# Optimization experiments

Hardware: AMD Instinct MI355X
Metric: run time of the kernel (lower is better)

## Reference

```python
import jax, jax.numpy as jnp
import numpy as np

B, S, I, H, O = 128, 512, 1024, 1024, 1024


def setup_inputs() -> dict:
    key = jax.random.key(0)
    ks = jax.random.split(key, 11)
    s = 0.02  # small init scale to keep exp/log-gate math stable
    return {
        "x": jax.random.normal(ks[0], (B, S, I), dtype=jnp.float32),
        "Wf": jax.random.normal(ks[1], (I + H, H), dtype=jnp.float32) * s,
        "bf": jax.random.normal(ks[2], (H,), dtype=jnp.float32) * s,
        "Wi": jax.random.normal(ks[3], (I + H, H), dtype=jnp.float32) * s,
        "bi": jax.random.normal(ks[4], (H,), dtype=jnp.float32) * s,
        "Wc": jax.random.normal(ks[5], (I + H, H), dtype=jnp.float32) * s,
        "bc": jax.random.normal(ks[6], (H,), dtype=jnp.float32) * s,
        "Wo": jax.random.normal(ks[7], (I + H, H), dtype=jnp.float32) * s,
        "bo": jax.random.normal(ks[8], (H,), dtype=jnp.float32) * s,
        "Wout": jax.random.normal(ks[9], (H, O), dtype=jnp.float32) * s,
        "bout": jax.random.normal(ks[10], (O,), dtype=jnp.float32) * s,
    }


def reference(x, Wf, bf, Wi, bi, Wc, bc, Wo, bo, Wout, bout):
    batch, seq_len, _ = x.shape
    hid = Wf.shape[1]

    def step(carry, x_t):
        h, c, n, m = carry  # each [B, H]
        comb = jnp.concatenate([x_t, h], axis=1)  # [B, I+H]
        f_log = comb @ Wf + bf
        i_log = comb @ Wi + bi
        m_new = jnp.maximum(f_log + m, i_log)  # stabilizer
        i_t = jnp.exp(i_log - m_new)
        f_t = jnp.exp(f_log + m - m_new)
        c_hat = jnp.tanh(comb @ Wc + bc)
        o_t = jax.nn.sigmoid(comb @ Wo + bo)
        c_new = f_t * c + i_t * c_hat
        n_new = f_t * n + i_t
        h_new = o_t * (c_new / (n_new + 1e-8))
        out = h_new @ Wout + bout  # [B, O]
        return (h_new, c_new, n_new, m_new), out

    init = tuple(jnp.zeros((batch, hid), x.dtype) for _ in range(4))
    (h, c, n, m), outs = jax.lax.scan(step, init, jnp.swapaxes(x, 0, 1))
    outputs = jnp.swapaxes(outs, 0, 1)  # [B, S, O]
    return outputs, h, c, n, m
```

## Files before the change

### kernel.cpp

```cpp
#include <hip/hip_runtime.h>
#include <cstddef>

#define B_ 128
#define S_ 512
#define I_ 1024
#define H_ 1024
#define G4_ 4096

typedef __attribute__((ext_vector_type(8))) short bf16x8;
typedef __attribute__((ext_vector_type(4))) float f32x4;
typedef unsigned short u16;
typedef unsigned int   u32;

__device__ inline u16 bf16_rn(float x) {
  return (u16)((__float_as_uint(x) + 0x8000u) >> 16);
}
__device__ inline u16 bf16_hi_rem(float x, float& rem) {
  const u32 hb = (__float_as_uint(x) + 0x8000u) & 0xFFFF0000u;
  rem = x - __uint_as_float(hb);
  return (u16)(hb >> 16);
}

__global__ __launch_bounds__(256) void k_zero(float* __restrict__ p, int n) {
  int i = blockIdx.x * 256 + threadIdx.x;
  if (i < n) p[i] = 0.0f;
}

__global__ __launch_bounds__(256) void k_wt(
    const float* __restrict__ Wf, const float* __restrict__ Wi,
    const float* __restrict__ Wc, const float* __restrict__ Wo,
    float* __restrict__ WT)
{
  const int gid = blockIdx.x * 256 + threadIdx.x;
  const int j4 = gid >> 12;
  const int s  = gid & 4095;
  const int ki = s >> 6, g = (s >> 4) & 3, kq = s & 15;
  const int k  = kq * 64 + ki;
  const float* Wg = (g == 0) ? Wf : (g == 1) ? Wi : (g == 2) ? Wc : Wo;
  const float4 v = *(const float4*)(Wg + (size_t)(I_ + k) * H_ + j4 * 4);
  *(float4*)(WT + (size_t)gid * 4) = v;
}

__global__ __launch_bounds__(256) void k_tr(
    const float* __restrict__ Wf, const float* __restrict__ Wi,
    const float* __restrict__ Wc, const float* __restrict__ Wo,
    const float* __restrict__ Wout,
    u16* __restrict__ Wxt_hi, u16* __restrict__ Wxt_lo,
    u16* __restrict__ Wot_hi, u16* __restrict__ Wot_lo)
{
  __shared__ float T_[64][65];
  const int kt = blockIdx.x, jt = blockIdx.y, z = blockIdx.z;
  const float* src = (z == 0) ? Wf : (z == 1) ? Wi : (z == 2) ? Wc
                     : (z == 3) ? Wo : Wout;
  u16* dh = (z < 4) ? Wxt_hi : Wot_hi;
  u16* dl = (z < 4) ? Wxt_lo : Wot_lo;
  const int nbase = (z < 4) ? (z * 1024 + jt * 64) : (jt * 64);
  const int tid = threadIdx.x;

#pragma unroll
  for (int it = 0; it < 4; ++it) {
    const int idx = it * 1024 + tid * 4;
    const int a = idx >> 6, c = idx & 63;
    const float4 v = *(const float4*)(src + (size_t)(kt * 64 + a) * 1024 + jt * 64 + c);
    T_[a][c] = v.x; T_[a][c + 1] = v.y; T_[a][c + 2] = v.z; T_[a][c + 3] = v.w;
  }
  __syncthreads();
#pragma unroll
  for (int it = 0; it < 16; ++it) {
    const int idx = it * 256 + tid;
    const int j = idx >> 6, k = idx & 63;
    const float xv = T_[k][j];
    float rem;
    const u16 hi = bf16_hi_rem(xv, rem);
    const u16 lo = bf16_rn(rem);
    const size_t o = (size_t)(nbase + j) * 1024 + kt * 64 + k;
    dh[o] = hi; dl[o] = lo;
  }
}

__global__ __launch_bounds__(256) void k_bias(
    const float* __restrict__ b0, const float* __restrict__ b1,
    const float* __restrict__ b2, const float* __restrict__ b3,
    float* __restrict__ b4)
{
  const int i = blockIdx.x * 256 + threadIdx.x;
  const int g = i >> 10;
  const float* s = (g == 0) ? b0 : (g == 1) ? b1 : (g == 2) ? b2 : b3;
  b4[i] = s[i & 1023];
}

__global__ __launch_bounds__(256) void k_xsplit(
    const float* __restrict__ x, u16* __restrict__ xh, u16* __restrict__ xl, int t0)
{
  const int id = blockIdx.x * 256 + threadIdx.x;
  const int tl = blockIdx.y;
  const int b  = id >> 7;
  const int k8 = (id & 127) << 3;
  const float* s = x + ((size_t)b * 512 + (size_t)(t0 + tl)) * 1024 + k8;
  const float4 v0 = *(const float4*)(s);
  const float4 v1 = *(const float4*)(s + 4);
  const float vs[8] = {v0.x, v0.y, v0.z, v0.w, v1.x, v1.y, v1.z, v1.w};
  u32 hw[4], lw[4];
#pragma unroll
  for (int p = 0; p < 4; ++p) {
    float r0, r1;
    const u16 h0 = bf16_hi_rem(vs[2 * p], r0);
    const u16 h1 = bf16_hi_rem(vs[2 * p + 1], r1);
    hw[p] = (u32)h0 | ((u32)h1 << 16);
    lw[p] = (u32)bf16_rn(r0) | ((u32)bf16_rn(r1) << 16);
  }
  const size_t o = ((size_t)tl * 128 + b) * 1024 + k8;
  *(uint4*)(xh + o) = make_uint4(hw[0], hw[1], hw[2], hw[3]);
  *(uint4*)(xl + o) = make_uint4(lw[0], lw[1], lw[2], lw[3]);
}

template<int MODE>
__global__ __launch_bounds__(256) void k_gemm_mfma(
    const u16* __restrict__ Ahg, const u16* __restrict__ Alg,
    const u16* __restrict__ Bhg, const u16* __restrict__ Blg,
    const float* __restrict__ bias,
    float* __restrict__ C, int t0)
{
  __shared__ u16 Ah[4096], Al[4096], Bh[4096], Bl[4096];
  const int tid = threadIdx.x;
  const int n0  = blockIdx.x * 128;
  const int by  = blockIdx.y;

  const int w = tid >> 6, lane = tid & 63;
  const int wm = w >> 1, wn = w & 1;
  const int lr = lane & 15, lh = lane >> 4;

  f32x4 acc[4][4];
#pragma unroll
  for (int mi = 0; mi < 4; ++mi)
#pragma unroll
    for (int ni = 0; ni < 4; ++ni) acc[mi][ni] = (f32x4){0.f, 0.f, 0.f, 0.f};

  const int srow  = tid >> 1;
  const int sb    = (tid & 1) * 2;
  const int swz   = (srow >> 1) & 3;
  const int l0 = srow * 32 + ((sb ^ swz) << 3);
  const int l1 = srow * 32 + (((sb + 1) ^ swz) << 3);
  const size_t ga = (size_t)(by * 128 + srow) * 1024 + (sb << 3);
  const size_t gb = (size_t)(n0 + srow) * 1024 + (sb << 3);

  int aoff[4], boff[4];
#pragma unroll
  for (int mi = 0; mi < 4; ++mi) {
    const int R = wm * 64 + mi * 16 + lr;
    aoff[mi] = R * 32 + ((lh ^ ((R >> 1) & 3)) << 3);
  }
#pragma unroll
  for (int ni = 0; ni < 4; ++ni) {
    const int Rn = wn * 64 + ni * 16 + lr;
    boff[ni] = Rn * 32 + ((lh ^ ((Rn >> 1) & 3)) << 3);
  }

  for (int k0 = 0; k0 < 1024; k0 += 32) {
    const uint4 vah0 = *(const uint4*)(Ahg + ga + k0);
    const uint4 vah1 = *(const uint4*)(Ahg + ga + k0 + 8);
    const uint4 vbh0 = *(const uint4*)(Bhg + gb + k0);
    const uint4 vbh1 = *(const uint4*)(Bhg + gb + k0 + 8);
    uint4 val0, val1, vbl0, vbl1;
    if (MODE == 0) {
      val0 = *(const uint4*)(Alg + ga + k0);
      val1 = *(const uint4*)(Alg + ga + k0 + 8);
      vbl0 = *(const uint4*)(Blg + gb + k0);
      vbl1 = *(const uint4*)(Blg + gb + k0 + 8);
    }
    __syncthreads();
    *(uint4*)(Ah + l0) = vah0; *(uint4*)(Ah + l1) = vah1;
    *(uint4*)(Bh + l0) = vbh0; *(uint4*)(Bh + l1) = vbh1;
    if (MODE == 0) {
      *(uint4*)(Al + l0) = val0; *(uint4*)(Al + l1) = val1;
      *(uint4*)(Bl + l0) = vbl0; *(uint4*)(Bl + l1) = vbl1;
    }
    __syncthreads();

    bf16x8 ahf[4], alf[4];
#pragma unroll
    for (int mi = 0; mi < 4; ++mi) {
      ahf[mi] = *(const bf16x8*)(&Ah[aoff[mi]]);
      if (MODE == 0) alf[mi] = *(const bf16x8*)(&Al[aoff[mi]]);
    }
#pragma unroll
    for (int ni = 0; ni < 4; ++ni) {
      const bf16x8 bhf = *(const bf16x8*)(&Bh[boff[ni]]);
      bf16x8 blf;
      if (MODE == 0) blf = *(const bf16x8*)(&Bl[boff[ni]]);
#pragma unroll
      for (int mi = 0; mi < 4; ++mi) {
        acc[mi][ni] = __builtin_amdgcn_mfma_f32_16x16x32_bf16(ahf[mi], bhf, acc[mi][ni], 0, 0, 0);
        if (MODE == 0) {
          acc[mi][ni] = __builtin_amdgcn_mfma_f32_16x16x32_bf16(ahf[mi], blf, acc[mi][ni], 0, 0, 0);
          acc[mi][ni] = __builtin_amdgcn_mfma_f32_16x16x32_bf16(alf[mi], bhf, acc[mi][ni], 0, 0, 0);
        }
      }
    }
  }

#pragma unroll
  for (int ni = 0; ni < 4; ++ni) {
    const int n = n0 + wn * 64 + ni * 16 + lr;
    const float bv = bias[n];
#pragma unroll
    for (int mi = 0; mi < 4; ++mi) {
      const int rb = wm * 64 + mi * 16 + lh * 4;
#pragma unroll
      for (int q = 0; q < 4; ++q) {
        const int r = rb + q;
        const float v = acc[mi][ni][q] + bv;
        if (MODE == 0) C[((size_t)by * 128 + r) * 4096 + n] = v;
        else           C[((size_t)r * 512 + (size_t)(t0 + by)) * 1024 + n] = v;
      }
    }
  }
}

__global__ __launch_bounds__(512) void k_step2(
    const float* __restrict__ WT,
    const float* __restrict__ preC,
    const float* __restrict__ hT_in,
    float* __restrict__ hT_out,
    float* __restrict__ cb, float* __restrict__ nb, float* __restrict__ mb,
    u16* __restrict__ hAllH,
    int t_local)
{
  __shared__ float Wl[16384];
  const int tid = threadIdx.x;
  const int bid = blockIdx.x;
  const int j0  = bid * 4;

  const int w    = tid >> 6;
  const int lane = tid & 63;
  const int kq   = lane & 15;
  const int bq   = lane >> 4;
  const int b0   = w * 16 + bq * 4;

  const int jj = kq & 3, ib = kq >> 2;
  const int bc = b0 + ib;
  const int jc = j0 + jj;
  const int sIdx = jc * 128 + bc;

  const float* pre_t = preC + (size_t)t_local * (128 * 4096) + (size_t)bc * 4096 + jc;
  const float pf = pre_t[0];
  const float pi = pre_t[1024];
  const float pc = pre_t[2048];
  const float po = pre_t[3072];
  const float m_old = mb[sIdx];
  const float c_old = cb[sIdx];
  const float n_old = nb[sIdx];

  const float* wt = WT + (size_t)bid * 16384;
#pragma unroll
  for (int r = 0; r < 8; ++r) {
    const int idx = r * 512 + tid;
    *(float4*)(&Wl[idx * 4]) = *(const float4*)(wt + (size_t)idx * 4);
  }
  __syncthreads();

  float acc[4][16];
#pragma unroll
  for (int i = 0; i < 4; ++i)
#pragma unroll
    for (int c = 0; c < 16; ++c) acc[i][c] = 0.0f;

  const float* hbase = hT_in + (size_t)kq * (64 * 128) + b0;
  const float* wb0   = &Wl[kq * 4];

  float4 h_c = *(const float4*)(hbase);
  float4 h_n = *(const float4*)(hbase + 128);
  float4 wA = *(const float4*)(wb0 + 0);
  float4 wB = *(const float4*)(wb0 + 64);
  float4 wC = *(const float4*)(wb0 + 128);
  float4 wD = *(const float4*)(wb0 + 192);

#pragma unroll 2
  for (int ki = 0; ki < 64; ++ki) {
    const int kin = (ki + 1) & 63;
    const int ki2 = (ki + 2) & 63;
    const float4 h_p = *(const float4*)(hbase + ki2 * 128);
    const float4 nA = *(const float4*)(wb0 + kin * 256 + 0);
    const float4 nB = *(const float4*)(wb0 + kin * 256 + 64);
    const float4 nC = *(const float4*)(wb0 + kin * 256 + 128);
    const float4 nD = *(const float4*)(wb0 + kin * 256 + 192);
    const float av[4] = {h_c.x, h_c.y, h_c.z, h_c.w};
    const float wv[16] = {wA.x, wA.y, wA.z, wA.w, wB.x, wB.y, wB.z, wB.w,
                          wC.x, wC.y, wC.z, wC.w, wD.x, wD.y, wD.z, wD.w};
#pragma unroll
    for (int i = 0; i < 4; ++i)
#pragma unroll
      for (int c = 0; c < 16; ++c)
        acc[i][c] = fmaf(av[i], wv[c], acc[i][c]);
    h_c = h_n; h_n = h_p;
    wA = nA; wB = nB; wC = nC; wD = nD;
  }

#pragma unroll
  for (int i = 0; i < 4; ++i)
#pragma unroll
    for (int c = 0; c < 16; ++c) {
      float v = acc[i][c];
      v += __shfl_xor(v, 1);
      v += __shfl_xor(v, 2);
      v += __shfl_xor(v, 4);
      v += __shfl_xor(v, 8);
      acc[i][c] = v;
    }

  float f_in, i_in, cc_in, o_in;
#define PICK_CASE(KQ) \
  case KQ: f_in = acc[(KQ) >> 2][(KQ) & 3];        \
           i_in = acc[(KQ) >> 2][4 + ((KQ) & 3)];  \
           cc_in = acc[(KQ) >> 2][8 + ((KQ) & 3)]; \
           o_in = acc[(KQ) >> 2][12 + ((KQ) & 3)]; break;
  switch (kq) {
    PICK_CASE(0)  PICK_CASE(1)  PICK_CASE(2)  PICK_CASE(3)
    PICK_CASE(4)  PICK_CASE(5)  PICK_CASE(6)  PICK_CASE(7)
    PICK_CASE(8)  PICK_CASE(9)  PICK_CASE(10) PICK_CASE(11)
    PICK_CASE(12) PICK_CASE(13) PICK_CASE(14) PICK_CASE(15)
    default: f_in = i_in = cc_in = o_in = 0.0f; break;
  }
#undef PICK_CASE

  const float f_log = f_in + pf;
  const float i_log = i_in + pi;
  const float c_log = cc_in + pc;
  const float o_log = o_in + po;

  const float m_new = fmaxf(f_log + m_old, i_log);
  const float i_t   = expf(i_log - m_new);
  const float f_t   = expf(f_log + m_old - m_new);
  const float c_hat = tanhf(c_log);
  const float o_t   = 1.0f / (1.0f + expf(-o_log));
  const float c_new = f_t * c_old + i_t * c_hat;
  const float n_new = f_t * n_old + i_t;
  const float h_new = o_t * (c_new / (n_new + 1e-8f));

  cb[sIdx] = c_new;
  nb[sIdx] = n_new;
  mb[sIdx] = m_new;
  hT_out[sIdx] = h_new;
  hAllH[((size_t)t_local * 128 + bc) * 1024 + jc] = bf16_rn(h_new);
}

__global__ __launch_bounds__(256) void k_tail(
    const float* __restrict__ hT, const float* __restrict__ cbp,
    const float* __restrict__ nbp, const float* __restrict__ mbp,
    float* __restrict__ dst)
{
  const int gid = blockIdx.x * 256 + threadIdx.x;
  const int q = gid >> 17, rem = gid & 131071;
  const int b = rem >> 10, j = rem & 1023;
  const float* src = (q == 0) ? hT : (q == 1) ? cbp : (q == 2) ? nbp : mbp;
  dst[gid] = src[j * B_ + b];
}

extern "C" void kernel_launch(void* const* d_in, const int* in_sizes, int n_in,
                              void* d_out, int out_size, void* d_ws, size_t ws_size,
                              hipStream_t stream) {
  const float* x    = (const float*)d_in[0];
  const float* Wf   = (const float*)d_in[1];
  const float* bfv  = (const float*)d_in[2];
  const float* Wi   = (const float*)d_in[3];
  const float* biv  = (const float*)d_in[4];
  const float* Wc   = (const float*)d_in[5];
  const float* bcv  = (const float*)d_in[6];
  const float* Wo   = (const float*)d_in[7];
  const float* bov  = (const float*)d_in[8];
  const float* Wout = (const float*)d_in[9];
  const float* bout = (const float*)d_in[10];
  float* out = (float*)d_out;

  float* hT0 = (float*)d_ws;
  float* hT1 = hT0 + 131072;
  float* cb  = hT0 + 2 * 131072;
  float* nb  = hT0 + 3 * 131072;
  float* mb  = hT0 + 4 * 131072;
  float* WT  = hT0 + 5 * 131072;
  u16* Wxt_hi = (u16*)(WT + 4194304);
  u16* Wxt_lo = Wxt_hi + 4194304;
  u16* Wot_hi = Wxt_lo + 4194304;
  u16* Wot_lo = Wot_hi + 1048576;
  float* bias4  = (float*)(Wot_lo + 1048576);
  float* chunk0 = bias4 + 4096;

  const size_t fixedF = (size_t)5 * 131072 + 4194304
                      + 4194304
                      + 1048576
                      + 4096;
  const size_t perTF = (size_t)128 * 4096 + 3 * 65536;
  const size_t availF = (ws_size / 4 > fixedF) ? (ws_size / 4 - fixedF) : 0;
  int Tc = (int)(availF / perTF);
  if (Tc > S_) Tc = S_;
  if (Tc < 1)  Tc = 1;

  float* preC   = chunk0;
  u16*   xs_hi  = (u16*)(preC + (size_t)Tc * 524288);
  u16*   xs_lo  = xs_hi + (size_t)Tc * 131072;
  u16*   hAll_h = xs_lo + (size_t)Tc * 131072;

  k_zero<<<2560, 256, 0, stream>>>(hT0, 5 * 131072);
  k_wt<<<4096, 256, 0, stream>>>(Wf, Wi, Wc, Wo, WT);
  k_tr<<<dim3(16, 16, 5), 256, 0, stream>>>(Wf, Wi, Wc, Wo, Wout,
                                            Wxt_hi, Wxt_lo, Wot_hi, Wot_lo);
  k_bias<<<16, 256, 0, stream>>>(bfv, biv, bcv, bov, bias4);

  for (int t0 = 0; t0 < S_; t0 += Tc) {
    const int T = (S_ - t0 < Tc) ? (S_ - t0) : Tc;

    k_xsplit<<<dim3(64, T), 256, 0, stream>>>(x, xs_hi, xs_lo, t0);
    k_gemm_mfma<0><<<dim3(32, T), 256, 0, stream>>>(xs_hi, xs_lo, Wxt_hi, Wxt_lo,
                                                    bias4, preC, t0);
    for (int tl = 0; tl < T; ++tl) {
      const int tg = t0 + tl;
      const float* hin = (tg & 1) ? hT1 : hT0;
      float* hout      = (tg & 1) ? hT0 : hT1;
      k_step2<<<256, 512, 0, stream>>>(WT, preC, hin, hout,
                                       cb, nb, mb, hAll_h, tl);
    }
    k_gemm_mfma<1><<<dim3(8, T), 256, 0, stream>>>(hAll_h, hAll_h, Wot_hi, Wot_hi,
                                                   bout, out, t0);
  }

  k_tail<<<2048, 256, 0, stream>>>(hT0, cb, nb, mb, out + (size_t)B_ * S_ * H_);
}
```

Measured before the change: 16.59 ms.

## Replace FP32 recurrent step with split-bf16 MFMA and gate-interleaved weights

The per-timestep recurrent matmul (h @ W_h) moves from scalar FP32 FMA over weights staged in LDS to bf16 MFMA instructions. Three products (hi*hi, hi*lo, lo*hi) approximate FP32 accuracy. Weights are pre-split into hi/lo bf16 and interleaved by gate so each output column group holds f,i,c,o together, and the bias layout is changed to match. The hidden state is double-buffered as hi/lo bf16, and gates are gathered with lane shuffles. Precision drops slightly because the lo*lo term is omitted, and each block now reads its weights straight from global/L2 every step instead of staging them in LDS.

```diff
diff --git a/kernel.cpp b/kernel.cpp
--- a/kernel.cpp
+++ b/kernel.cpp
@@ -26,42 +26,29 @@
   if (i < n) p[i] = 0.0f;
 }
 
-__global__ __launch_bounds__(256) void k_wt(
-    const float* __restrict__ Wf, const float* __restrict__ Wi,
-    const float* __restrict__ Wc, const float* __restrict__ Wo,
-    float* __restrict__ WT)
-{
-  const int gid = blockIdx.x * 256 + threadIdx.x;
-  const int j4 = gid >> 12;
-  const int s  = gid & 4095;
-  const int ki = s >> 6, g = (s >> 4) & 3, kq = s & 15;
-  const int k  = kq * 64 + ki;
-  const float* Wg = (g == 0) ? Wf : (g == 1) ? Wi : (g == 2) ? Wc : Wo;
-  const float4 v = *(const float4*)(Wg + (size_t)(I_ + k) * H_ + j4 * 4);
-  *(float4*)(WT + (size_t)gid * 4) = v;
-}
-
 __global__ __launch_bounds__(256) void k_tr(
     const float* __restrict__ Wf, const float* __restrict__ Wi,
     const float* __restrict__ Wc, const float* __restrict__ Wo,
     const float* __restrict__ Wout,
     u16* __restrict__ Wxt_hi, u16* __restrict__ Wxt_lo,
-    u16* __restrict__ Wot_hi, u16* __restrict__ Wot_lo)
+    u16* __restrict__ Wot_hi, u16* __restrict__ Wot_lo,
+    u16* __restrict__ Wht_hi, u16* __restrict__ Wht_lo)
 {
   __shared__ float T_[64][65];
   const int kt = blockIdx.x, jt = blockIdx.y, z = blockIdx.z;
-  const float* src = (z == 0) ? Wf : (z == 1) ? Wi : (z == 2) ? Wc
-                     : (z == 3) ? Wo : Wout;
-  u16* dh = (z < 4) ? Wxt_hi : Wot_hi;
-  u16* dl = (z < 4) ? Wxt_lo : Wot_lo;
-  const int nbase = (z < 4) ? (z * 1024 + jt * 64) : (jt * 64);
+  const int g = (z < 4) ? z : (z - 5);
+  const float* src = (z == 4) ? Wout
+                   : (g == 0) ? Wf : (g == 1) ? Wi : (g == 2) ? Wc : Wo;
+  u16* dh = (z < 4) ? Wxt_hi : (z == 4) ? Wot_hi : Wht_hi;
+  u16* dl = (z < 4) ? Wxt_lo : (z == 4) ? Wot_lo : Wht_lo;
+  const int rowbase = ((z >= 5) ? I_ : 0) + kt * 64;
   const int tid = threadIdx.x;
 
 #pragma unroll
   for (int it = 0; it < 4; ++it) {
     const int idx = it * 1024 + tid * 4;
     const int a = idx >> 6, c = idx & 63;
-    const float4 v = *(const float4*)(src + (size_t)(kt * 64 + a) * 1024 + jt * 64 + c);
+    const float4 v = *(const float4*)(src + (size_t)(rowbase + a) * 1024 + jt * 64 + c);
     T_[a][c] = v.x; T_[a][c + 1] = v.y; T_[a][c + 2] = v.z; T_[a][c + 3] = v.w;
   }
   __syncthreads();
@@ -73,7 +60,9 @@
     float rem;
     const u16 hi = bf16_hi_rem(xv, rem);
     const u16 lo = bf16_rn(rem);
-    const size_t o = (size_t)(nbase + j) * 1024 + kt * 64 + k;
+    size_t o;
+    if (z == 4) o = (size_t)(jt * 64 + j) * 1024 + kt * 64 + k;
+    else        o = ((size_t)(jt * 64 + j) * 4 + g) * 1024 + kt * 64 + k;
     dh[o] = hi; dl[o] = lo;
   }
 }
@@ -84,9 +73,9 @@
     float* __restrict__ b4)
 {
   const int i = blockIdx.x * 256 + threadIdx.x;
-  const int g = i >> 10;
+  const int g = i & 3, j = i >> 2;
   const float* s = (g == 0) ? b0 : (g == 1) ? b1 : (g == 2) ? b2 : b3;
-  b4[i] = s[i & 1023];
+  b4[i] = s[j];
 }
 
 __global__ __launch_bounds__(256) void k_xsplit(
@@ -217,116 +206,69 @@
   }
 }
 
-__global__ __launch_bounds__(512) void k_step2(
-    const float* __restrict__ WT,
+__global__ __launch_bounds__(512) void k_step3(
+    const u16* __restrict__ Whh, const u16* __restrict__ Whl,
     const float* __restrict__ preC,
-    const float* __restrict__ hT_in,
-    float* __restrict__ hT_out,
+    const u16* __restrict__ hIh, const u16* __restrict__ hIl,
+    u16* __restrict__ hOh, u16* __restrict__ hOl,
+    float* __restrict__ hT,
     float* __restrict__ cb, float* __restrict__ nb, float* __restrict__ mb,
     u16* __restrict__ hAllH,
     int t_local)
 {
-  __shared__ float Wl[16384];
   const int tid = threadIdx.x;
   const int bid = blockIdx.x;
-  const int j0  = bid * 4;
-
-  const int w    = tid >> 6;
-  const int lane = tid & 63;
-  const int kq   = lane & 15;
-  const int bq   = lane >> 4;
-  const int b0   = w * 16 + bq * 4;
-
-  const int jj = kq & 3, ib = kq >> 2;
-  const int bc = b0 + ib;
-  const int jc = j0 + jj;
-  const int sIdx = jc * 128 + bc;
-
-  const float* pre_t = preC + (size_t)t_local * (128 * 4096) + (size_t)bc * 4096 + jc;
-  const float pf = pre_t[0];
-  const float pi = pre_t[1024];
-  const float pc = pre_t[2048];
-  const float po = pre_t[3072];
+  const int jt = bid >> 2, mq = bid & 3;
+  const int w = tid >> 6, lane = tid & 63;
+  const int mi = w & 1, nf = w >> 1;
+  const int lr = lane & 15, lh = lane >> 4;
+  const int rowb = mq * 32 + mi * 16;
+
+  const int G = lr & 3;
+  const int j = jt * 16 + nf * 4 + (lr >> 2);
+  const int b = rowb + lh * 4 + G;
+  const int sIdx = j * 128 + b;
+
+  const float4 pre4 = *(const float4*)(preC + (size_t)t_local * (128 * 4096)
+                                       + (size_t)b * 4096 + j * 4);
   const float m_old = mb[sIdx];
   const float c_old = cb[sIdx];
   const float n_old = nb[sIdx];
 
-  const float* wt = WT + (size_t)bid * 16384;
-#pragma unroll
-  for (int r = 0; r < 8; ++r) {
-    const int idx = r * 512 + tid;
-    *(float4*)(&Wl[idx * 4]) = *(const float4*)(wt + (size_t)idx * 4);
-  }
-  __syncthreads();
-
-  float acc[4][16];
-#pragma unroll
-  for (int i = 0; i < 4; ++i)
-#pragma unroll
-    for (int c = 0; c < 16; ++c) acc[i][c] = 0.0f;
-
-  const float* hbase = hT_in + (size_t)kq * (64 * 128) + b0;
-  const float* wb0   = &Wl[kq * 4];
-
-  float4 h_c = *(const float4*)(hbase);
-  float4 h_n = *(const float4*)(hbase + 128);
-  float4 wA = *(const float4*)(wb0 + 0);
-  float4 wB = *(const float4*)(wb0 + 64);
-  float4 wC = *(const float4*)(wb0 + 128);
-  float4 wD = *(const float4*)(wb0 + 192);
-
-#pragma unroll 2
-  for (int ki = 0; ki < 64; ++ki) {
-    const int kin = (ki + 1) & 63;
-    const int ki2 = (ki + 2) & 63;
-    const float4 h_p = *(const float4*)(hbase + ki2 * 128);
-    const float4 nA = *(const float4*)(wb0 + kin * 256 + 0);
-    const float4 nB = *(const float4*)(wb0 + kin * 256 + 64);
-    const float4 nC = *(const float4*)(wb0 + kin * 256 + 128);
-    const float4 nD = *(const float4*)(wb0 + kin * 256 + 192);
-    const float av[4] = {h_c.x, h_c.y, h_c.z, h_c.w};
-    const float wv[16] = {wA.x, wA.y, wA.z, wA.w, wB.x, wB.y, wB.z, wB.w,
-                          wC.x, wC.y, wC.z, wC.w, wD.x, wD.y, wD.z, wD.w};
-#pragma unroll
-    for (int i = 0; i < 4; ++i)
-#pragma unroll
-      for (int c = 0; c < 16; ++c)
-        acc[i][c] = fmaf(av[i], wv[c], acc[i][c]);
-    h_c = h_n; h_n = h_p;
-    wA = nA; wB = nB; wC = nC; wD = nD;
-  }
-
-#pragma unroll
-  for (int i = 0; i < 4; ++i)
-#pragma unroll
-    for (int c = 0; c < 16; ++c) {
-      float v = acc[i][c];
-      v += __shfl_xor(v, 1);
-      v += __shfl_xor(v, 2);
-      v += __shfl_xor(v, 4);
-      v += __shfl_xor(v, 8);
-      acc[i][c] = v;
-    }
-
-  float f_in, i_in, cc_in, o_in;
-#define PICK_CASE(KQ) \
-  case KQ: f_in = acc[(KQ) >> 2][(KQ) & 3];        \
-           i_in = acc[(KQ) >> 2][4 + ((KQ) & 3)];  \
-           cc_in = acc[(KQ) >> 2][8 + ((KQ) & 3)]; \
-           o_in = acc[(KQ) >> 2][12 + ((KQ) & 3)]; break;
-  switch (kq) {
-    PICK_CASE(0)  PICK_CASE(1)  PICK_CASE(2)  PICK_CASE(3)
-    PICK_CASE(4)  PICK_CASE(5)  PICK_CASE(6)  PICK_CASE(7)
-    PICK_CASE(8)  PICK_CASE(9)  PICK_CASE(10) PICK_CASE(11)
-    PICK_CASE(12) PICK_CASE(13) PICK_CASE(14) PICK_CASE(15)
-    default: f_in = i_in = cc_in = o_in = 0.0f; break;
-  }
-#undef PICK_CASE
-
-  const float f_log = f_in + pf;
-  const float i_log = i_in + pi;
-  const float c_log = cc_in + pc;
-  const float o_log = o_in + po;
+  const u16* aH = hIh + (size_t)(rowb + lr) * 1024 + lh * 8;
+  const u16* aL = hIl + (size_t)(rowb + lr) * 1024 + lh * 8;
+  const u16* bH = Whh + (size_t)(jt * 64 + nf * 16 + lr) * 1024 + lh * 8;
+  const u16* bL = Whl + (size_t)(jt * 64 + nf * 16 + lr) * 1024 + lh * 8;
+
+  f32x4 acc = {0.f, 0.f, 0.f, 0.f};
+#pragma unroll 4
+  for (int k0 = 0; k0 < 1024; k0 += 32) {
+    const bf16x8 ah = *(const bf16x8*)(aH + k0);
+    const bf16x8 al = *(const bf16x8*)(aL + k0);
+    const bf16x8 bh = *(const bf16x8*)(bH + k0);
+    const bf16x8 bl = *(const bf16x8*)(bL + k0);
+    acc = __builtin_amdgcn_mfma_f32_16x16x32_bf16(ah, bh, acc, 0, 0, 0);
+    acc = __builtin_amdgcn_mfma_f32_16x16x32_bf16(ah, bl, acc, 0, 0, 0);
+    acc = __builtin_amdgcn_mfma_f32_16x16x32_bf16(al, bh, acc, 0, 0, 0);
+  }
+
+  const float a0 = acc[0], a1 = acc[1], a2 = acc[2], a3 = acc[3];
+  const float s10 = __shfl_xor(a0, 1), s11 = __shfl_xor(a1, 1),
+              s12 = __shfl_xor(a2, 1), s13 = __shfl_xor(a3, 1);
+  const float s20 = __shfl_xor(a0, 2), s21 = __shfl_xor(a1, 2),
+              s22 = __shfl_xor(a2, 2), s23 = __shfl_xor(a3, 2);
+  const float s30 = __shfl_xor(a0, 3), s31 = __shfl_xor(a1, 3),
+              s32 = __shfl_xor(a2, 3), s33 = __shfl_xor(a3, 3);
+  float fv, iv, cv, ov;
+  if      (G == 0) { fv = a0;  iv = s10; cv = s20; ov = s30; }
+  else if (G == 1) { fv = s11; iv = a1;  cv = s31; ov = s21; }
+  else if (G == 2) { fv = s22; iv = s32; cv = a2;  ov = s12; }
+  else             { fv = s33; iv = s23; cv = s13; ov = a3;  }
+
+  const float f_log = fv + pre4.x;
+  const float i_log = iv + pre4.y;
+  const float c_log = cv + pre4.z;
+  const float o_log = ov + pre4.w;
 
   const float m_new = fmaxf(f_log + m_old, i_log);
   const float i_t   = expf(i_log - m_new);
@@ -340,8 +282,14 @@
   cb[sIdx] = c_new;
   nb[sIdx] = n_new;
   mb[sIdx] = m_new;
-  hT_out[sIdx] = h_new;
-  hAllH[((size_t)t_local * 128 + bc) * 1024 + jc] = bf16_rn(h_new);
+  hT[sIdx] = h_new;
+
+  float rem;
+  const u16 hh = bf16_hi_rem(h_new, rem);
+  const u16 hl = bf16_rn(rem);
+  hOh[(size_t)b * 1024 + j] = hh;
+  hOl[(size_t)b * 1024 + j] = hl;
+  hAllH[((size_t)t_local * 128 + b) * 1024 + j] = hh;
 }
 
 __global__ __launch_bounds__(256) void k_tail(
@@ -372,38 +320,50 @@
   const float* bout = (const float*)d_in[10];
   float* out = (float*)d_out;
 
-  float* hT0 = (float*)d_ws;
-  float* hT1 = hT0 + 131072;
-  float* cb  = hT0 + 2 * 131072;
-  float* nb  = hT0 + 3 * 131072;
-  float* mb  = hT0 + 4 * 131072;
-  float* WT  = hT0 + 5 * 131072;
-  u16* Wxt_hi = (u16*)(WT + 4194304);
+  float* base = (float*)d_ws;
+  float* hT = base;
+  float* cb = base + 131072;
+  float* nb = base + 2 * 131072;
+  float* mb = base + 3 * 131072;
+  u16* hH0h = (u16*)(base + 4 * 131072);
+  u16* hH0l = hH0h + 131072;
+  u16* hH1h = hH0l + 131072;
+  u16* hH1l = hH1h + 131072;
+  u16* Wxt_hi = (u16*)(base + 6 * 131072);
   u16* Wxt_lo = Wxt_hi + 4194304;
-  u16* Wot_hi = Wxt_lo + 4194304;
+  u16* Wht_hi = Wxt_lo + 4194304;
+  u16* Wht_lo = Wht_hi + 4194304;
+  u16* Wot_hi = Wht_lo + 4194304;
   u16* Wot_lo = Wot_hi + 1048576;
   float* bias4  = (float*)(Wot_lo + 1048576);
   float* chunk0 = bias4 + 4096;
 
-  const size_t fixedF = (size_t)5 * 131072 + 4194304
-                      + 4194304
-                      + 1048576
-                      + 4096;
+  const size_t fixedF = (size_t)6 * 131072
+                      + 4 * 2097152
+                      + 2 * 524288 / 2 * 2
+                      ;
+  const size_t fixedF2 = (size_t)6 * 131072
+                       + ((size_t)4 * 4194304 + 2 * 1048576) / 2
+                       + 4096;
   const size_t perTF = (size_t)128 * 4096 + 3 * 65536;
-  const size_t availF = (ws_size / 4 > fixedF) ? (ws_size / 4 - fixedF) : 0;
+  const size_t availF = (ws_size / 4 > fixedF2) ? (ws_size / 4 - fixedF2) : 0;
   int Tc = (int)(availF / perTF);
   if (Tc > S_) Tc = S_;
   if (Tc < 1)  Tc = 1;
+  (void)fixedF;
 
   float* preC   = chunk0;
   u16*   xs_hi  = (u16*)(preC + (size_t)Tc * 524288);
   u16*   xs_lo  = xs_hi + (size_t)Tc * 131072;
   u16*   hAll_h = xs_lo + (size_t)Tc * 131072;
 
-  k_zero<<<2560, 256, 0, stream>>>(hT0, 5 * 131072);
-  k_wt<<<4096, 256, 0, stream>>>(Wf, Wi, Wc, Wo, WT);
-  k_tr<<<dim3(16, 16, 5), 256, 0, stream>>>(Wf, Wi, Wc, Wo, Wout,
-                                            Wxt_hi, Wxt_lo, Wot_hi, Wot_lo);
+  u16* hHi[2] = {hH0h, hH1h};
+  u16* hLo[2] = {hH0l, hH1l};
+
+  k_zero<<<2048, 256, 0, stream>>>(cb, 4 * 131072);
+  k_tr<<<dim3(16, 16, 9), 256, 0, stream>>>(Wf, Wi, Wc, Wo, Wout,
+                                            Wxt_hi, Wxt_lo, Wot_hi, Wot_lo,
+                                            Wht_hi, Wht_lo);
   k_bias<<<16, 256, 0, stream>>>(bfv, biv, bcv, bov, bias4);
 
   for (int t0 = 0; t0 < S_; t0 += Tc) {
@@ -414,14 +374,14 @@
                                                     bias4, preC, t0);
     for (int tl = 0; tl < T; ++tl) {
       const int tg = t0 + tl;
-      const float* hin = (tg & 1) ? hT1 : hT0;
-      float* hout      = (tg & 1) ? hT0 : hT1;
-      k_step2<<<256, 512, 0, stream>>>(WT, preC, hin, hout,
-                                       cb, nb, mb, hAll_h, tl);
+      const int ri = tg & 1, wi = ri ^ 1;
+      k_step3<<<256, 512, 0, stream>>>(Wht_hi, Wht_lo, preC,
+                                       hHi[ri], hLo[ri], hHi[wi], hLo[wi],
+                                       hT, cb, nb, mb, hAll_h, tl);
     }
     k_gemm_mfma<1><<<dim3(8, T), 256, 0, stream>>>(hAll_h, hAll_h, Wot_hi, Wot_hi,
                                                    bout, out, t0);
   }
 
-  k_tail<<<2048, 256, 0, stream>>>(hT0, cb, nb, mb, out + (size_t)B_ * S_ * H_);
-}
+  k_tail<<<2048, 256, 0, stream>>>(hT, cb, nb, mb, out + (size_t)B_ * S_ * H_);
+}
```

New measurement: 19.53 ms. 17.7% more time.
